# Optimization experiments

Measured on AMD Instinct MI355X. Metric: run time of the kernel, lower is better.

## Reference

```python
import jax, jax.numpy as jnp
import numpy as np

T, B, N, DEG = 2048, 8192, 64, 5
MAX_I = 100.0      # max_current
MAX_FR = 200.0     # max_firing_rate


def poly_act(z, poly_coeff, g_b):
    # z: [B, 1] -> PolynomialActivation forward
    x = (z - g_b) / MAX_I                                   # [B, 1]
    powers = jnp.concatenate([x ** k for k in range(DEG + 1)], axis=-1)  # [B, DEG+1]
    poly = powers @ (poly_coeff ** 2)[:, None]              # [B, 1]
    return jax.nn.relu(MAX_FR * jnp.tanh(poly))


def setup_inputs() -> dict:
    key = jax.random.key(0)
    ks = jax.random.split(key, 7)
    return {
        "currents": jax.random.normal(ks[0], (T, B), jnp.float32),
        "fs0": jnp.zeros((B,), jnp.float32),
        "a": jax.random.uniform(ks[1], (N,), jnp.float32),
        "b": jax.random.uniform(ks[2], (N,), jnp.float32) * 1e-3,
        "w": jax.random.uniform(ks[3], (N, 1), jnp.float32) / N,
        "ds": jax.random.uniform(ks[4], (N,), jnp.float32, 0.05, 0.95),
        "poly_coeff": jax.random.uniform(ks[5], (DEG + 1,), jnp.float32) * 0.3,
        "g_b": jnp.zeros((), jnp.float32),
    }


def reference(currents, fs0, a, b, w, ds, poly_coeff, g_b):
    # currents: [T, B]; recurrence over T time bins (FiringRateModel.forward per step)
    def step(carry, cur_t):
        v, f = carry
        # v <- (1 - ds) * v + outer(currents, a) + 1000 * outer(fs, b)
        v = (1.0 - ds) * v + cur_t[:, None] * a + 1000.0 * f[:, None] * b  # [B, N]
        f = poly_act(v @ w, poly_coeff, g_b)[:, 0]                          # [B]
        return (v, f), f

    v0 = jnp.zeros((currents.shape[1], ds.shape[0]), currents.dtype)
    _, fs = jax.lax.scan(step, (v0, fs0), currents)
    return fs  # [T, B]
```

## Files before the change

kernel.cpp:

```cpp
#include <hip/hip_runtime.h>


#define TT 2048
#define BB 8192

typedef float v2f __attribute__((ext_vector_type(2)));

__device__ __forceinline__ float dpp_add_x1(float z) {
    float o;
    asm("v_add_f32 %0, %1, %2 quad_perm:[1,0,3,2] row_mask:0xf bank_mask:0xf"
        : "=v"(o) : "v"(z), "v"(z));
    return o;
}
__device__ __forceinline__ float dpp_add_x2(float z) {
    float o;
    asm("v_add_f32 %0, %1, %2 quad_perm:[2,3,0,1] row_mask:0xf bank_mask:0xf"
        : "=v"(o) : "v"(z), "v"(z));
    return o;
}
__device__ __forceinline__ float dpp_add_r8(float z) {
    float o;
    asm("v_add_f32 %0, %1, %2 row_ror:8 row_mask:0xf bank_mask:0xf"
        : "=v"(o) : "v"(z), "v"(z));
    return o;
}
__device__ __forceinline__ float allreduce8(float z) {
    z = dpp_add_x1(z);
    z = dpp_add_x2(z);
    z = dpp_add_r8(z);
    return z;
}

__device__ __forceinline__ float bfi_keep(unsigned mk, float nf, float of) {
    unsigned r = (__float_as_uint(nf) & mk) | (__float_as_uint(of) & ~mk);
    return __uint_as_float(r);
}

#define STEP(ccur, cnext, so, FIN, FOUT) do {                           \
    v2f f2 = { FIN, FIN };                                              \
    v2f c2 = { (ccur), (ccur) };                                        \
    sg0 = __builtin_elementwise_fma(d0, sg0,                            \
            __builtin_elementwise_fma(c2, A0, f2 * B0));                \
    sg1 = __builtin_elementwise_fma(d1, sg1,                            \
            __builtin_elementwise_fma(c2, A1, f2 * B1));                \
    sg2 = __builtin_elementwise_fma(d2, sg2,                            \
            __builtin_elementwise_fma(c2, A2, f2 * B2));                \
    sg3 = __builtin_elementwise_fma(d3, sg3,                            \
            __builtin_elementwise_fma(c2, A3, f2 * B3));                \
    v2f ss = (sg0 + sg1) + (sg2 + sg3);                                 \
    float Sr = allreduce8(ss.x + ss.y);                                 \
    float base = fmaf((cnext), SAp, Sr);                                \
    float x2 = yy * yy;                                                 \
    float t1 = fmaf(q5, yy, q4);                                        \
    float t2 = fmaf(q3, yy, q2);                                        \
    float t3 = fmaf(q1, yy, q0);                                        \
    float pl = fmaf(t1, x2, t2);                                        \
    pl = fmaf(pl, x2, t3);                                              \
    pl = fminf(pl, 0.0f);                    \
    float ee = __builtin_amdgcn_exp2f(pl);                              \
    FOUT = fmaf(__builtin_amdgcn_rcpf(1.0f + ee), 400.0f, -200.0f);     \
    yy = fmaf(FOUT, SBp, base);                                         \
    fkeep = bfi_keep(msk[(so) & 7], FOUT, fkeep);                       \
} while (0)

#define FLUSH() do {                                                    \
    *optr = fkeep;                                                      \
    optr += 8 * BB;                                                     \
} while (0)

__global__ __launch_bounds__(256, 1) void frm_kernel(
    const float* __restrict__ cur, const float* __restrict__ fs0,
    const float* __restrict__ av,  const float* __restrict__ bv,
    const float* __restrict__ wv,  const float* __restrict__ dsv,
    const float* __restrict__ pcv, const float* __restrict__ gbv,
    float* __restrict__ outp)
{
    const int tid  = blockIdx.x * 256 + threadIdx.x;
    const int lane = threadIdx.x & 15;
    const int row  = tid >> 4;
    const int sub  = (lane >> 2) & 1;
    const int chain = row * 2 + sub;
    const int h    = ((lane >> 3) << 2) | (lane & 3);

    const int n0 = h * 8;
    float wk0 = wv[n0+0], wk1 = wv[n0+1], wk2 = wv[n0+2], wk3 = wv[n0+3];
    float wk4 = wv[n0+4], wk5 = wv[n0+5], wk6 = wv[n0+6], wk7 = wv[n0+7];
    float dk0 = 1.0f-dsv[n0+0], dk1 = 1.0f-dsv[n0+1], dk2 = 1.0f-dsv[n0+2], dk3 = 1.0f-dsv[n0+3];
    float dk4 = 1.0f-dsv[n0+4], dk5 = 1.0f-dsv[n0+5], dk6 = 1.0f-dsv[n0+6], dk7 = 1.0f-dsv[n0+7];
    float ak0 = 0.01f*av[n0+0]*wk0, ak1 = 0.01f*av[n0+1]*wk1;
    float ak2 = 0.01f*av[n0+2]*wk2, ak3 = 0.01f*av[n0+3]*wk3;
    float ak4 = 0.01f*av[n0+4]*wk4, ak5 = 0.01f*av[n0+5]*wk5;
    float ak6 = 0.01f*av[n0+6]*wk6, ak7 = 0.01f*av[n0+7]*wk7;
    float bk0 = 10.0f*bv[n0+0]*wk0, bk1 = 10.0f*bv[n0+1]*wk1;
    float bk2 = 10.0f*bv[n0+2]*wk2, bk3 = 10.0f*bv[n0+3]*wk3;
    float bk4 = 10.0f*bv[n0+4]*wk4, bk5 = 10.0f*bv[n0+5]*wk5;
    float bk6 = 10.0f*bv[n0+6]*wk6, bk7 = 10.0f*bv[n0+7]*wk7;

    const v2f d0 = {dk0, dk1}, d1 = {dk2, dk3}, d2 = {dk4, dk5}, d3 = {dk6, dk7};
    const v2f A0 = {dk0*ak0, dk1*ak1}, A1 = {dk2*ak2, dk3*ak3};
    const v2f A2 = {dk4*ak4, dk5*ak5}, A3 = {dk6*ak6, dk7*ak7};
    const v2f B0 = {dk0*bk0, dk1*bk1}, B1 = {dk2*bk2, dk3*bk3};
    const v2f B2 = {dk4*bk4, dk5*bk5}, B3 = {dk6*bk6, dk7*bk7};

    const float SAp = allreduce8(((ak0+ak1)+(ak2+ak3)) + ((ak4+ak5)+(ak6+ak7)));
    const float SBp = allreduce8(((bk0+bk1)+(bk2+bk3)) + ((bk4+bk5)+(bk6+bk7)));

    const float M = -2.8853900817779268f;
    float c0 = M*pcv[0]*pcv[0], c1 = M*pcv[1]*pcv[1], c2c = M*pcv[2]*pcv[2];
    float c3 = M*pcv[3]*pcv[3], c4 = M*pcv[4]*pcv[4], c5 = M*pcv[5]*pcv[5];
    const float s = -gbv[0] * 0.01f;
    {
        c4 = fmaf(c5, s, c4); c3 = fmaf(c4, s, c3); c2c = fmaf(c3, s, c2c);
        c1 = fmaf(c2c, s, c1); c0 = fmaf(c1, s, c0);
        c4 = fmaf(c5, s, c4); c3 = fmaf(c4, s, c3); c2c = fmaf(c3, s, c2c);
        c1 = fmaf(c2c, s, c1);
        c4 = fmaf(c5, s, c4); c3 = fmaf(c4, s, c3); c2c = fmaf(c3, s, c2c);
        c4 = fmaf(c5, s, c4); c3 = fmaf(c4, s, c3);
        c4 = fmaf(c5, s, c4);
    }
    const float q0 = c0, q1 = c1, q2 = c2c, q3 = c3, q4 = c4, q5 = c5;

    unsigned msk[8];
#pragma unroll
    for (int k = 0; k < 8; ++k) msk[k] = (h == k) ? 0xFFFFFFFFu : 0u;

    float fA = fs0[chain];
    float fB;
    float fkeep = 0.0f;
    v2f sg0 = {0,0}, sg1 = {0,0}, sg2 = {0,0}, sg3 = {0,0};

    const float* cpt = cur + chain;
    float* optr = outp + chain + h * BB;

    float P0 = cpt[0*BB], P1 = cpt[1*BB], P2 = cpt[2*BB], P3 = cpt[3*BB];
    float P4 = cpt[4*BB], P5 = cpt[5*BB], P6 = cpt[6*BB], P7 = cpt[7*BB];
    float Q0 = cpt[8*BB], Q1 = cpt[9*BB], Q2 = cpt[10*BB], Q3 = cpt[11*BB];
    float Q4 = cpt[12*BB], Q5 = cpt[13*BB], Q6 = cpt[14*BB], Q7 = cpt[15*BB];

    float yy = fmaf(fA, SBp, P0 * SAp);

    int obase = 0;
    for (int t = 0; t + 32 <= TT; t += 16) {
        STEP(P0, P1, 0, fA, fB);  STEP(P1, P2, 1, fB, fA);
        STEP(P2, P3, 2, fA, fB);  STEP(P3, P4, 3, fB, fA);
        STEP(P4, P5, 4, fA, fB);  STEP(P5, P6, 5, fB, fA);
        STEP(P6, P7, 6, fA, fB);  STEP(P7, Q0, 7, fB, fA);
        FLUSH();
        P0 = cpt[obase + 16*BB]; P1 = cpt[obase + 17*BB];
        P2 = cpt[obase + 18*BB]; P3 = cpt[obase + 19*BB];
        P4 = cpt[obase + 20*BB]; P5 = cpt[obase + 21*BB];
        P6 = cpt[obase + 22*BB]; P7 = cpt[obase + 23*BB];
        STEP(Q0, Q1, 8, fA, fB);  STEP(Q1, Q2, 9, fB, fA);
        STEP(Q2, Q3, 10, fA, fB); STEP(Q3, Q4, 11, fB, fA);
        STEP(Q4, Q5, 12, fA, fB); STEP(Q5, Q6, 13, fB, fA);
        STEP(Q6, Q7, 14, fA, fB); STEP(Q7, P0, 15, fB, fA);
        FLUSH();
        Q0 = cpt[obase + 24*BB]; Q1 = cpt[obase + 25*BB];
        Q2 = cpt[obase + 26*BB]; Q3 = cpt[obase + 27*BB];
        Q4 = cpt[obase + 28*BB]; Q5 = cpt[obase + 29*BB];
        Q6 = cpt[obase + 30*BB]; Q7 = cpt[obase + 31*BB];
        obase += 16 * BB;
    }
    STEP(P0, P1, 0, fA, fB);  STEP(P1, P2, 1, fB, fA);
    STEP(P2, P3, 2, fA, fB);  STEP(P3, P4, 3, fB, fA);
    STEP(P4, P5, 4, fA, fB);  STEP(P5, P6, 5, fB, fA);
    STEP(P6, P7, 6, fA, fB);  STEP(P7, Q0, 7, fB, fA);
    FLUSH();
    STEP(Q0, Q1, 8, fA, fB);  STEP(Q1, Q2, 9, fB, fA);
    STEP(Q2, Q3, 10, fA, fB); STEP(Q3, Q4, 11, fB, fA);
    STEP(Q4, Q5, 12, fA, fB); STEP(Q5, Q6, 13, fB, fA);
    STEP(Q6, Q7, 14, fA, fB); STEP(Q7, 0.0f, 15, fB, fA);
    FLUSH();
}

extern "C" void kernel_launch(void* const* d_in, const int* in_sizes, int n_in,
                              void* d_out, int out_size, void* d_ws, size_t ws_size,
                              hipStream_t stream) {
    const float* cur = (const float*)d_in[0];
    const float* fs0 = (const float*)d_in[1];
    const float* a   = (const float*)d_in[2];
    const float* b   = (const float*)d_in[3];
    const float* w   = (const float*)d_in[4];
    const float* ds  = (const float*)d_in[5];
    const float* pc  = (const float*)d_in[6];
    const float* gb  = (const float*)d_in[7];
    float* out = (float*)d_out;

    const int threads = 256;
    const int grid = (BB * 8) / threads;
    frm_kernel<<<grid, threads, 0, stream>>>(cur, fs0, a, b, w, ds, pc, gb, out);
}
```

Measured before the change: 168.2 us.

## Split each chain's hidden dimension over 16 lanes instead of 8

Each batch chain is now handled by 16 lanes, each holding 4 of the 64 hidden units, instead of 8 lanes holding 8 each. The per-step reduction gains a row_ror:4 DPP stage, the output mask and flush cover 16 time steps, the grid doubles, and launch bounds allow 2 blocks per CU. The aim is to halve the per-lane FMA work on the serial recurrence critical path and raise occupancy to hide latency, at the cost of an extra DPP add per step and twice as many threads redundantly running the scalar polynomial and activation chain.

```diff
diff --git a/kernel.cpp b/kernel.cpp
--- a/kernel.cpp
+++ b/kernel.cpp
@@ -18,15 +18,22 @@
         : "=v"(o) : "v"(z), "v"(z));
     return o;
 }
+__device__ __forceinline__ float dpp_add_r4(float z) {
+    float o;
+    asm("v_add_f32 %0, %1, %2 row_ror:4 row_mask:0xf bank_mask:0xf"
+        : "=v"(o) : "v"(z), "v"(z));
+    return o;
+}
 __device__ __forceinline__ float dpp_add_r8(float z) {
     float o;
     asm("v_add_f32 %0, %1, %2 row_ror:8 row_mask:0xf bank_mask:0xf"
         : "=v"(o) : "v"(z), "v"(z));
     return o;
 }
-__device__ __forceinline__ float allreduce8(float z) {
+__device__ __forceinline__ float allreduce16(float z) {
     z = dpp_add_x1(z);
     z = dpp_add_x2(z);
+    z = dpp_add_r4(z);
     z = dpp_add_r8(z);
     return z;
 }
@@ -43,12 +50,8 @@
             __builtin_elementwise_fma(c2, A0, f2 * B0));                \
     sg1 = __builtin_elementwise_fma(d1, sg1,                            \
             __builtin_elementwise_fma(c2, A1, f2 * B1));                \
-    sg2 = __builtin_elementwise_fma(d2, sg2,                            \
-            __builtin_elementwise_fma(c2, A2, f2 * B2));                \
-    sg3 = __builtin_elementwise_fma(d3, sg3,                            \
-            __builtin_elementwise_fma(c2, A3, f2 * B3));                \
-    v2f ss = (sg0 + sg1) + (sg2 + sg3);                                 \
-    float Sr = allreduce8(ss.x + ss.y);                                 \
+    v2f ss = sg0 + sg1;                                                 \
+    float Sr = allreduce16(ss.x + ss.y);                                \
     float base = fmaf((cnext), SAp, Sr);                                \
     float x2 = yy * yy;                                                 \
     float t1 = fmaf(q5, yy, q4);                                        \
@@ -60,50 +63,40 @@
     float ee = __builtin_amdgcn_exp2f(pl);                              \
     FOUT = fmaf(__builtin_amdgcn_rcpf(1.0f + ee), 400.0f, -200.0f);     \
     yy = fmaf(FOUT, SBp, base);                                         \
-    fkeep = bfi_keep(msk[(so) & 7], FOUT, fkeep);                       \
+    fkeep = bfi_keep(msk[(so) & 15], FOUT, fkeep);                      \
 } while (0)
 
 #define FLUSH() do {                                                    \
     *optr = fkeep;                                                      \
-    optr += 8 * BB;                                                     \
+    optr += 16 * BB;                                                    \
 } while (0)
 
-__global__ __launch_bounds__(256, 1) void frm_kernel(
+__global__ __launch_bounds__(256, 2) void frm_kernel(
     const float* __restrict__ cur, const float* __restrict__ fs0,
     const float* __restrict__ av,  const float* __restrict__ bv,
     const float* __restrict__ wv,  const float* __restrict__ dsv,
     const float* __restrict__ pcv, const float* __restrict__ gbv,
     float* __restrict__ outp)
 {
-    const int tid  = blockIdx.x * 256 + threadIdx.x;
-    const int lane = threadIdx.x & 15;
-    const int row  = tid >> 4;
-    const int sub  = (lane >> 2) & 1;
-    const int chain = row * 2 + sub;
-    const int h    = ((lane >> 3) << 2) | (lane & 3);
+    const int tid   = blockIdx.x * 256 + threadIdx.x;
+    const int chain = tid >> 4;
+    const int g     = threadIdx.x & 15;
 
-    const int n0 = h * 8;
-    float wk0 = wv[n0+0], wk1 = wv[n0+1], wk2 = wv[n0+2], wk3 = wv[n0+3];
-    float wk4 = wv[n0+4], wk5 = wv[n0+5], wk6 = wv[n0+6], wk7 = wv[n0+7];
-    float dk0 = 1.0f-dsv[n0+0], dk1 = 1.0f-dsv[n0+1], dk2 = 1.0f-dsv[n0+2], dk3 = 1.0f-dsv[n0+3];
-    float dk4 = 1.0f-dsv[n0+4], dk5 = 1.0f-dsv[n0+5], dk6 = 1.0f-dsv[n0+6], dk7 = 1.0f-dsv[n0+7];
-    float ak0 = 0.01f*av[n0+0]*wk0, ak1 = 0.01f*av[n0+1]*wk1;
-    float ak2 = 0.01f*av[n0+2]*wk2, ak3 = 0.01f*av[n0+3]*wk3;
-    float ak4 = 0.01f*av[n0+4]*wk4, ak5 = 0.01f*av[n0+5]*wk5;
-    float ak6 = 0.01f*av[n0+6]*wk6, ak7 = 0.01f*av[n0+7]*wk7;
-    float bk0 = 10.0f*bv[n0+0]*wk0, bk1 = 10.0f*bv[n0+1]*wk1;
-    float bk2 = 10.0f*bv[n0+2]*wk2, bk3 = 10.0f*bv[n0+3]*wk3;
-    float bk4 = 10.0f*bv[n0+4]*wk4, bk5 = 10.0f*bv[n0+5]*wk5;
-    float bk6 = 10.0f*bv[n0+6]*wk6, bk7 = 10.0f*bv[n0+7]*wk7;
+    const int n0 = g * 4;
+    const float w0 = wv[n0+0], w1 = wv[n0+1], w2 = wv[n0+2], w3 = wv[n0+3];
+    const float dk0 = 1.0f - dsv[n0+0], dk1 = 1.0f - dsv[n0+1];
+    const float dk2 = 1.0f - dsv[n0+2], dk3 = 1.0f - dsv[n0+3];
+    const float ak0 = 0.01f*av[n0+0]*w0, ak1 = 0.01f*av[n0+1]*w1;
+    const float ak2 = 0.01f*av[n0+2]*w2, ak3 = 0.01f*av[n0+3]*w3;
+    const float bk0 = 10.0f*bv[n0+0]*w0, bk1 = 10.0f*bv[n0+1]*w1;
+    const float bk2 = 10.0f*bv[n0+2]*w2, bk3 = 10.0f*bv[n0+3]*w3;
 
-    const v2f d0 = {dk0, dk1}, d1 = {dk2, dk3}, d2 = {dk4, dk5}, d3 = {dk6, dk7};
+    const v2f d0 = {dk0, dk1}, d1 = {dk2, dk3};
     const v2f A0 = {dk0*ak0, dk1*ak1}, A1 = {dk2*ak2, dk3*ak3};
-    const v2f A2 = {dk4*ak4, dk5*ak5}, A3 = {dk6*ak6, dk7*ak7};
     const v2f B0 = {dk0*bk0, dk1*bk1}, B1 = {dk2*bk2, dk3*bk3};
-    const v2f B2 = {dk4*bk4, dk5*bk5}, B3 = {dk6*bk6, dk7*bk7};
 
-    const float SAp = allreduce8(((ak0+ak1)+(ak2+ak3)) + ((ak4+ak5)+(ak6+ak7)));
-    const float SBp = allreduce8(((bk0+bk1)+(bk2+bk3)) + ((bk4+bk5)+(bk6+bk7)));
+    const float SAp = allreduce16((ak0+ak1)+(ak2+ak3));
+    const float SBp = allreduce16((bk0+bk1)+(bk2+bk3));
 
     const float M = -2.8853900817779268f;
     float c0 = M*pcv[0]*pcv[0], c1 = M*pcv[1]*pcv[1], c2c = M*pcv[2]*pcv[2];
@@ -120,17 +113,17 @@
     }
     const float q0 = c0, q1 = c1, q2 = c2c, q3 = c3, q4 = c4, q5 = c5;
 
-    unsigned msk[8];
+    unsigned msk[16];
 #pragma unroll
-    for (int k = 0; k < 8; ++k) msk[k] = (h == k) ? 0xFFFFFFFFu : 0u;
+    for (int k = 0; k < 16; ++k) msk[k] = (g == k) ? 0xFFFFFFFFu : 0u;
 
     float fA = fs0[chain];
     float fB;
     float fkeep = 0.0f;
-    v2f sg0 = {0,0}, sg1 = {0,0}, sg2 = {0,0}, sg3 = {0,0};
+    v2f sg0 = {0,0}, sg1 = {0,0};
 
     const float* cpt = cur + chain;
-    float* optr = outp + chain + h * BB;
+    float* optr = outp + chain + g * BB;
 
     float P0 = cpt[0*BB], P1 = cpt[1*BB], P2 = cpt[2*BB], P3 = cpt[3*BB];
     float P4 = cpt[4*BB], P5 = cpt[5*BB], P6 = cpt[6*BB], P7 = cpt[7*BB];
@@ -145,7 +138,6 @@
         STEP(P2, P3, 2, fA, fB);  STEP(P3, P4, 3, fB, fA);
         STEP(P4, P5, 4, fA, fB);  STEP(P5, P6, 5, fB, fA);
         STEP(P6, P7, 6, fA, fB);  STEP(P7, Q0, 7, fB, fA);
-        FLUSH();
         P0 = cpt[obase + 16*BB]; P1 = cpt[obase + 17*BB];
         P2 = cpt[obase + 18*BB]; P3 = cpt[obase + 19*BB];
         P4 = cpt[obase + 20*BB]; P5 = cpt[obase + 21*BB];
@@ -165,7 +157,6 @@
     STEP(P2, P3, 2, fA, fB);  STEP(P3, P4, 3, fB, fA);
     STEP(P4, P5, 4, fA, fB);  STEP(P5, P6, 5, fB, fA);
     STEP(P6, P7, 6, fA, fB);  STEP(P7, Q0, 7, fB, fA);
-    FLUSH();
     STEP(Q0, Q1, 8, fA, fB);  STEP(Q1, Q2, 9, fB, fA);
     STEP(Q2, Q3, 10, fA, fB); STEP(Q3, Q4, 11, fB, fA);
     STEP(Q4, Q5, 12, fA, fB); STEP(Q5, Q6, 13, fB, fA);
@@ -187,6 +178,6 @@
     float* out = (float*)d_out;
 
     const int threads = 256;
-    const int grid = (BB * 8) / threads;
+    const int grid = (BB * 16) / threads;
     frm_kernel<<<grid, threads, 0, stream>>>(cur, fs0, a, b, w, ds, pc, gb, out);
 }
```

Result: slower. 239.9 us (+42.7%).

## Unroll recurrence two steps so cross-lane reduction runs off the critical path

Applied to the files above, without the earlier changes.

Rewrites the linear state recurrence so each step's reduction uses the previous state sums, with coefficients pre-multiplied by the squared decay. Two extra scalar terms carry the current and previous inputs and firing rate. This lets the DPP allreduce overlap with the polynomial/exp/rcp chain instead of sitting serially between the state update and the activation, shortening the per-step dependency latency. It adds a few scalar FMAs per step and changes floating-point summation order slightly.

```diff
diff --git a/kernel.cpp b/kernel.cpp
--- a/kernel.cpp
+++ b/kernel.cpp
@@ -37,29 +37,39 @@
 }
 
 #define STEP(ccur, cnext, so, FIN, FOUT) do {                           \
+    v2f ssa = sg0 + sg1;                   \
+    v2f ssb = sg2 + sg3;                                                \
     v2f f2 = { FIN, FIN };                                              \
     v2f c2 = { (ccur), (ccur) };                                        \
-    sg0 = __builtin_elementwise_fma(d0, sg0,                            \
-            __builtin_elementwise_fma(c2, A0, f2 * B0));                \
-    sg1 = __builtin_elementwise_fma(d1, sg1,                            \
-            __builtin_elementwise_fma(c2, A1, f2 * B1));                \
-    sg2 = __builtin_elementwise_fma(d2, sg2,                            \
-            __builtin_elementwise_fma(c2, A2, f2 * B2));                \
-    sg3 = __builtin_elementwise_fma(d3, sg3,                            \
-            __builtin_elementwise_fma(c2, A3, f2 * B3));                \
-    v2f ss = (sg0 + sg1) + (sg2 + sg3);                                 \
-    float Sr = allreduce8(ss.x + ss.y);                                 \
-    float base = fmaf((cnext), SAp, Sr);                                \
+    float tot = (ccur) * U1p;                                           \
+    v2f u0 = __builtin_elementwise_fma(c2, A0, f2 * B0);                \
+    v2f u1 = __builtin_elementwise_fma(c2, A1, f2 * B1);                \
+    v2f ss = ssa + ssb;                                                 \
+    float s01 = ss.x + ss.y;                                            \
+    v2f u2 = __builtin_elementwise_fma(c2, A2, f2 * B2);                \
+    float r1 = dpp_add_x1(s01);                                         \
+    v2f u3 = __builtin_elementwise_fma(c2, A3, f2 * B3);                \
+    tot = fmaf((cnext), U0p, tot);                                      \
+    sg0 = __builtin_elementwise_fma(d0, sg0, u0);                       \
+    sg1 = __builtin_elementwise_fma(d1, sg1, u1);                       \
+    float r2 = dpp_add_x2(r1);                                          \
+    sg2 = __builtin_elementwise_fma(d2, sg2, u2);                       \
+    sg3 = __builtin_elementwise_fma(d3, sg3, u3);                       \
+    tot = fmaf(FIN, G1p, tot);                                          \
     float x2 = yy * yy;                                                 \
     float t1 = fmaf(q5, yy, q4);                                        \
     float t2 = fmaf(q3, yy, q2);                                        \
     float t3 = fmaf(q1, yy, q0);                                        \
+    float r3 = dpp_add_r8(r2);                                          \
     float pl = fmaf(t1, x2, t2);                                        \
     pl = fmaf(pl, x2, t3);                                              \
     pl = fminf(pl, 0.0f);                    \
     float ee = __builtin_amdgcn_exp2f(pl);                              \
-    FOUT = fmaf(__builtin_amdgcn_rcpf(1.0f + ee), 400.0f, -200.0f);     \
-    yy = fmaf(FOUT, SBp, base);                                         \
+    float base = r3 + tot;                                              \
+    float eo = 1.0f + ee;                                               \
+    float er = __builtin_amdgcn_rcpf(eo);                               \
+    FOUT = fmaf(er, 400.0f, -200.0f);                                   \
+    yy = fmaf(FOUT, G0p, base);                                         \
     fkeep = bfi_keep(msk[(so) & 7], FOUT, fkeep);                       \
 } while (0)
 
@@ -87,23 +97,27 @@
     float wk4 = wv[n0+4], wk5 = wv[n0+5], wk6 = wv[n0+6], wk7 = wv[n0+7];
     float dk0 = 1.0f-dsv[n0+0], dk1 = 1.0f-dsv[n0+1], dk2 = 1.0f-dsv[n0+2], dk3 = 1.0f-dsv[n0+3];
     float dk4 = 1.0f-dsv[n0+4], dk5 = 1.0f-dsv[n0+5], dk6 = 1.0f-dsv[n0+6], dk7 = 1.0f-dsv[n0+7];
-    float ak0 = 0.01f*av[n0+0]*wk0, ak1 = 0.01f*av[n0+1]*wk1;
-    float ak2 = 0.01f*av[n0+2]*wk2, ak3 = 0.01f*av[n0+3]*wk3;
-    float ak4 = 0.01f*av[n0+4]*wk4, ak5 = 0.01f*av[n0+5]*wk5;
-    float ak6 = 0.01f*av[n0+6]*wk6, ak7 = 0.01f*av[n0+7]*wk7;
-    float bk0 = 10.0f*bv[n0+0]*wk0, bk1 = 10.0f*bv[n0+1]*wk1;
-    float bk2 = 10.0f*bv[n0+2]*wk2, bk3 = 10.0f*bv[n0+3]*wk3;
-    float bk4 = 10.0f*bv[n0+4]*wk4, bk5 = 10.0f*bv[n0+5]*wk5;
-    float bk6 = 10.0f*bv[n0+6]*wk6, bk7 = 10.0f*bv[n0+7]*wk7;
+    float uk0 = 0.01f*av[n0+0]*wk0, uk1 = 0.01f*av[n0+1]*wk1;
+    float uk2 = 0.01f*av[n0+2]*wk2, uk3 = 0.01f*av[n0+3]*wk3;
+    float uk4 = 0.01f*av[n0+4]*wk4, uk5 = 0.01f*av[n0+5]*wk5;
+    float uk6 = 0.01f*av[n0+6]*wk6, uk7 = 0.01f*av[n0+7]*wk7;
+    float gk0 = 10.0f*bv[n0+0]*wk0, gk1 = 10.0f*bv[n0+1]*wk1;
+    float gk2 = 10.0f*bv[n0+2]*wk2, gk3 = 10.0f*bv[n0+3]*wk3;
+    float gk4 = 10.0f*bv[n0+4]*wk4, gk5 = 10.0f*bv[n0+5]*wk5;
+    float gk6 = 10.0f*bv[n0+6]*wk6, gk7 = 10.0f*bv[n0+7]*wk7;
 
     const v2f d0 = {dk0, dk1}, d1 = {dk2, dk3}, d2 = {dk4, dk5}, d3 = {dk6, dk7};
-    const v2f A0 = {dk0*ak0, dk1*ak1}, A1 = {dk2*ak2, dk3*ak3};
-    const v2f A2 = {dk4*ak4, dk5*ak5}, A3 = {dk6*ak6, dk7*ak7};
-    const v2f B0 = {dk0*bk0, dk1*bk1}, B1 = {dk2*bk2, dk3*bk3};
-    const v2f B2 = {dk4*bk4, dk5*bk5}, B3 = {dk6*bk6, dk7*bk7};
-
-    const float SAp = allreduce8(((ak0+ak1)+(ak2+ak3)) + ((ak4+ak5)+(ak6+ak7)));
-    const float SBp = allreduce8(((bk0+bk1)+(bk2+bk3)) + ((bk4+bk5)+(bk6+bk7)));
+    const v2f A0 = {dk0*dk0*uk0, dk1*dk1*uk1}, A1 = {dk2*dk2*uk2, dk3*dk3*uk3};
+    const v2f A2 = {dk4*dk4*uk4, dk5*dk5*uk5}, A3 = {dk6*dk6*uk6, dk7*dk7*uk7};
+    const v2f B0 = {dk0*dk0*gk0, dk1*dk1*gk1}, B1 = {dk2*dk2*gk2, dk3*dk3*gk3};
+    const v2f B2 = {dk4*dk4*gk4, dk5*dk5*gk5}, B3 = {dk6*dk6*gk6, dk7*dk7*gk7};
+
+    const float U0p = allreduce8(((uk0+uk1)+(uk2+uk3)) + ((uk4+uk5)+(uk6+uk7)));
+    const float U1p = allreduce8(((dk0*uk0+dk1*uk1)+(dk2*uk2+dk3*uk3))
+                               + ((dk4*uk4+dk5*uk5)+(dk6*uk6+dk7*uk7)));
+    const float G0p = allreduce8(((gk0+gk1)+(gk2+gk3)) + ((gk4+gk5)+(gk6+gk7)));
+    const float G1p = allreduce8(((dk0*gk0+dk1*gk1)+(dk2*gk2+dk3*gk3))
+                               + ((dk4*gk4+dk5*gk5)+(dk6*gk6+dk7*gk7)));
 
     const float M = -2.8853900817779268f;
     float c0 = M*pcv[0]*pcv[0], c1 = M*pcv[1]*pcv[1], c2c = M*pcv[2]*pcv[2];
@@ -137,7 +151,7 @@
     float Q0 = cpt[8*BB], Q1 = cpt[9*BB], Q2 = cpt[10*BB], Q3 = cpt[11*BB];
     float Q4 = cpt[12*BB], Q5 = cpt[13*BB], Q6 = cpt[14*BB], Q7 = cpt[15*BB];
 
-    float yy = fmaf(fA, SBp, P0 * SAp);
+    float yy = fmaf(fA, G0p, P0 * U0p);
 
     int obase = 0;
     for (int t = 0; t + 32 <= TT; t += 16) {
```

After: 176.5 us. 4.9% more time.
